# Kernel tuning notes

Measured on AMD Instinct MI355X. Metric: run time of the kernel, lower is better.

## Reference

```python
import jax, jax.numpy as jnp
import numpy as np

VOCAB_SIZE = 95
EMBED_DIM = 48
HIDDEN_DIM = 48


def setup_inputs() -> dict:
    key = jax.random.key(0)
    ks = jax.random.split(key, 8)
    B, S = 2048, 512
    x = jax.random.randint(ks[0], (B, S), 0, VOCAB_SIZE)
    s_e = 1.0  # torch Embedding default init ~ N(0,1); scale irrelevant for correctness
    emb = jax.random.normal(ks[1], (VOCAB_SIZE, EMBED_DIM), dtype=jnp.float32) * s_e
    k = 1.0 / np.sqrt(HIDDEN_DIM)
    w_ih = jax.random.uniform(ks[2], (3 * HIDDEN_DIM, EMBED_DIM), minval=-k, maxval=k, dtype=jnp.float32)
    w_hh = jax.random.uniform(ks[3], (3 * HIDDEN_DIM, HIDDEN_DIM), minval=-k, maxval=k, dtype=jnp.float32)
    b_ih = jax.random.uniform(ks[4], (3 * HIDDEN_DIM,), minval=-k, maxval=k, dtype=jnp.float32)
    b_hh = jax.random.uniform(ks[5], (3 * HIDDEN_DIM,), minval=-k, maxval=k, dtype=jnp.float32)
    w_out = jax.random.uniform(ks[6], (VOCAB_SIZE, HIDDEN_DIM), minval=-k, maxval=k, dtype=jnp.float32)
    b_out = jax.random.uniform(ks[7], (VOCAB_SIZE,), minval=-k, maxval=k, dtype=jnp.float32)
    return {"x": x, "emb": emb, "w_ih": w_ih, "w_hh": w_hh,
            "b_ih": b_ih, "b_hh": b_hh, "w_out": w_out, "b_out": b_out}


def _gru(embed, w_ih, w_hh, b_ih, b_hh):
    # embed: [B, S, E]. PyTorch GRU (single layer, batch_first):
    #   r = sig(Wir x + bir + Whr h + bhr); z = sig(Wiz x + biz + Whz h + bhz)
    B = embed.shape[0]
    H = w_hh.shape[1]
    # precompute input contributions for all timesteps: [S, B, 3H]
    xg = jnp.einsum('bse,ge->bsg', embed, w_ih) + b_ih
    xg = jnp.swapaxes(xg, 0, 1)
    h0 = jnp.zeros((B, H), dtype=embed.dtype)

    def step(h, xg_t):
        gh = h @ w_hh.T + b_hh  # [B, 3H]
        xr, xz, xn = jnp.split(xg_t, 3, axis=-1)
        hr, hz, hn = jnp.split(gh, 3, axis=-1)
        r = jax.nn.sigmoid(xr + hr)
        z = jax.nn.sigmoid(xz + hz)
        n = jnp.tanh(xn + r * hn)
        h_new = (1.0 - z) * n + z * h
        return h_new, h_new

    h_last, hs = jax.lax.scan(step, h0, xg)
    out = jnp.swapaxes(hs, 0, 1)  # [B, S, H]
    return out, h_last


def reference(x, emb, w_ih, w_hh, b_ih, b_hh, w_out, b_out):
    embed = emb[x]  # [B, S, E]
    out, h_last = _gru(embed, w_ih, w_hh, b_ih, b_hh)
    logits = jnp.einsum('bsh,vh->bsv', out, w_out) + b_out  # [B, S, V]
    hidden = h_last[None]  # [1, B, H] to match torch GRU hidden layout
    return logits, hidden
```

## Files before the change

### kernel.cpp

```cpp
#include <hip/hip_runtime.h>
#include <hip/hip_bf16.h>


#define BATCH 2048
#define SEQ   512
#define HDIM  48
#define VOCAB 95
#define G3    144

__device__ __forceinline__ float sigmoidf_(float x) {
    return 1.0f / (1.0f + __expf(-x));
}

__global__ void xg_precompute(const float* __restrict__ emb,
                              const float* __restrict__ w_ih,
                              const float* __restrict__ b_ih,
                              float* __restrict__ xg) {
    int v = blockIdx.x;
    int g = threadIdx.x;
    const float* e = emb + v * HDIM;
    const float* w = w_ih + g * HDIM;
    float a0 = 0.f, a1 = 0.f, a2 = 0.f, a3 = 0.f;
    #pragma unroll
    for (int k = 0; k < HDIM; k += 4) {
        a0 = fmaf(w[k + 0], e[k + 0], a0);
        a1 = fmaf(w[k + 1], e[k + 1], a1);
        a2 = fmaf(w[k + 2], e[k + 2], a2);
        a3 = fmaf(w[k + 3], e[k + 3], a3);
    }
    xg[v * G3 + g] = b_ih[g] + ((a0 + a1) + (a2 + a3));
}

__global__ __launch_bounds__(64, 2)
void gru_rec(const int* __restrict__ x,
             const float* __restrict__ xg_table,
             const float* __restrict__ w_hh,
             const float* __restrict__ b_hh,
             float* __restrict__ out,
             float* __restrict__ hidden) {
    const int row = blockIdx.x;
    const int j   = threadIdx.x;
    __shared__ float hsh[HDIM];

    float4 wr[12], wz[12], wn[12];
    float br = 0.f, bz = 0.f, bn = 0.f;
    float hj = 0.f;
    if (j < HDIM) {
        const float4* whr = (const float4*)(w_hh + (j         ) * HDIM);
        const float4* whz = (const float4*)(w_hh + (j +   HDIM) * HDIM);
        const float4* whn = (const float4*)(w_hh + (j + 2*HDIM) * HDIM);
        #pragma unroll
        for (int k = 0; k < 12; ++k) { wr[k] = whr[k]; wz[k] = whz[k]; wn[k] = whn[k]; }
        br = b_hh[j]; bz = b_hh[j + HDIM]; bn = b_hh[j + 2*HDIM];
        hsh[j] = 0.f;
    }
    __syncthreads();

    const int* xrow = x + row * SEQ;
    int tok = xrow[0];
    for (int t = 0; t < SEQ; ++t) {
        int tok_next = (t + 1 < SEQ) ? xrow[t + 1] : 0;
        float hnew = 0.f;
        if (j < HDIM) {
            const float* xg = xg_table + tok * G3;
            float xr = xg[j], xz = xg[j + HDIM], xn = xg[j + 2*HDIM];
            float accr = br, accz = bz, accn = bn;
            const float4* h4 = (const float4*)hsh;
            #pragma unroll
            for (int k = 0; k < 12; ++k) {
                float4 hh = h4[k];
                accr = fmaf(wr[k].x, hh.x, accr); accr = fmaf(wr[k].y, hh.y, accr);
                accr = fmaf(wr[k].z, hh.z, accr); accr = fmaf(wr[k].w, hh.w, accr);
                accz = fmaf(wz[k].x, hh.x, accz); accz = fmaf(wz[k].y, hh.y, accz);
                accz = fmaf(wz[k].z, hh.z, accz); accz = fmaf(wz[k].w, hh.w, accz);
                accn = fmaf(wn[k].x, hh.x, accn); accn = fmaf(wn[k].y, hh.y, accn);
                accn = fmaf(wn[k].z, hh.z, accn); accn = fmaf(wn[k].w, hh.w, accn);
            }
            float r = sigmoidf_(xr + accr);
            float z = sigmoidf_(xz + accz);
            float n = tanhf(xn + r * accn);
            hnew = (1.0f - z) * n + z * hj;
            hj = hnew;
            out[((long)(row * SEQ + t)) * VOCAB + j] = hnew;
        }
        __syncthreads();
        if (j < HDIM) hsh[j] = hnew;
        __syncthreads();
        tok = tok_next;
    }
    if (j < HDIM) hidden[row * HDIM + j] = hj;
}

__global__ __launch_bounds__(256, 2)
void logits_k(const float* __restrict__ w_out,
              const float* __restrict__ b_out,
              float* __restrict__ out) {
    __shared__ float hsh[256 * HDIM];
    const long pos0 = (long)blockIdx.x * 256;
    const int tid = threadIdx.x;

    for (int i = tid; i < 256 * HDIM; i += 256) {
        int p = i / HDIM;
        int k = i - p * HDIM;
        hsh[i] = out[(pos0 + p) * VOCAB + k];
    }
    __syncthreads();

    float h[HDIM];
    #pragma unroll
    for (int k = 0; k < 12; ++k)
        ((float4*)h)[k] = ((const float4*)(hsh + tid * HDIM))[k];

    float* orow = out + (pos0 + tid) * VOCAB;
    for (int v = 0; v < VOCAB; ++v) {
        const float* w = w_out + v * HDIM;
        float a0 = 0.f, a1 = 0.f, a2 = 0.f, a3 = 0.f;
        #pragma unroll
        for (int k = 0; k < HDIM; k += 4) {
            a0 = fmaf(w[k + 0], h[k + 0], a0);
            a1 = fmaf(w[k + 1], h[k + 1], a1);
            a2 = fmaf(w[k + 2], h[k + 2], a2);
            a3 = fmaf(w[k + 3], h[k + 3], a3);
        }
        orow[v] = b_out[v] + ((a0 + a1) + (a2 + a3));
    }
}

extern "C" void kernel_launch(void* const* d_in, const int* in_sizes, int n_in,
                              void* d_out, int out_size, void* d_ws, size_t ws_size,
                              hipStream_t stream) {
    const int*   x     = (const int*)d_in[0];
    const float* emb   = (const float*)d_in[1];
    const float* w_ih  = (const float*)d_in[2];
    const float* w_hh  = (const float*)d_in[3];
    const float* b_ih  = (const float*)d_in[4];
    const float* b_hh  = (const float*)d_in[5];
    const float* w_out = (const float*)d_in[6];
    const float* b_out = (const float*)d_in[7];

    float* out    = (float*)d_out;
    float* hidden = out + (long)BATCH * SEQ * VOCAB;
    float* xg     = (float*)d_ws;

    xg_precompute<<<VOCAB, G3, 0, stream>>>(emb, w_ih, b_ih, xg);
    gru_rec<<<BATCH, 64, 0, stream>>>(x, xg, w_hh, b_hh, out, hidden);
    logits_k<<<(BATCH * SEQ) / 256, 256, 0, stream>>>(w_out, b_out, out);
}
```

Baseline: 1.329 ms.

## Use wave barriers in GRU, prefetch gate inputs, tile logits with coalesced stores

The recurrent kernel, which runs a single 64-thread wave per row, now uses wave barriers instead of full block barriers. It also prefetches the next timestep's input-gate values ahead of the dependent recurrence math and swaps tanhf for an exp-based fast tanh. The logits kernel now processes 64 positions per block, with each wave computing a slice of the vocabulary. Results go to a shared-memory tile that is written back with coalesced float4 stores, replacing strided per-thread row writes. This risks more LDS use per block, and the fast tanh gives slightly different rounding.

```diff
diff --git a/kernel.cpp b/kernel.cpp
--- a/kernel.cpp
+++ b/kernel.cpp
@@ -7,9 +7,16 @@
 #define HDIM  48
 #define VOCAB 95
 #define G3    144
+#define HPAD  52
 
 __device__ __forceinline__ float sigmoidf_(float x) {
     return 1.0f / (1.0f + __expf(-x));
+}
+__device__ __forceinline__ float fast_tanh(float x) {
+    float ax = fabsf(x);
+    float e  = __expf(-2.0f * ax);
+    float r  = (1.0f - e) / (1.0f + e);
+    return copysignf(r, x);
 }
 
 __global__ void xg_precompute(const float* __restrict__ emb,
@@ -54,16 +61,26 @@
         br = b_hh[j]; bz = b_hh[j + HDIM]; bn = b_hh[j + 2*HDIM];
         hsh[j] = 0.f;
     }
-    __syncthreads();
+    __builtin_amdgcn_wave_barrier();
 
     const int* xrow = x + row * SEQ;
-    int tok = xrow[0];
+    float* orow = out + (long)row * SEQ * VOCAB + j;
+
+    int tok0 = xrow[0];
+    float xr = 0.f, xz = 0.f, xn = 0.f;
+    if (j < HDIM) {
+        const float* xg0 = xg_table + tok0 * G3;
+        xr = xg0[j]; xz = xg0[j + HDIM]; xn = xg0[j + 2*HDIM];
+    }
+
     for (int t = 0; t < SEQ; ++t) {
         int tok_next = (t + 1 < SEQ) ? xrow[t + 1] : 0;
+        const float* xgn = xg_table + tok_next * G3;
+        float xr_n = 0.f, xz_n = 0.f, xn_n = 0.f;
+        if (j < HDIM) { xr_n = xgn[j]; xz_n = xgn[j + HDIM]; xn_n = xgn[j + 2*HDIM]; }
+
         float hnew = 0.f;
         if (j < HDIM) {
-            const float* xg = xg_table + tok * G3;
-            float xr = xg[j], xz = xg[j + HDIM], xn = xg[j + 2*HDIM];
             float accr = br, accz = bz, accn = bn;
             const float4* h4 = (const float4*)hsh;
             #pragma unroll
@@ -78,52 +95,64 @@
             }
             float r = sigmoidf_(xr + accr);
             float z = sigmoidf_(xz + accz);
-            float n = tanhf(xn + r * accn);
+            float n = fast_tanh(xn + r * accn);
             hnew = (1.0f - z) * n + z * hj;
             hj = hnew;
-            out[((long)(row * SEQ + t)) * VOCAB + j] = hnew;
+            orow[(long)t * VOCAB] = hnew;
         }
-        __syncthreads();
+        __builtin_amdgcn_wave_barrier();
         if (j < HDIM) hsh[j] = hnew;
-        __syncthreads();
-        tok = tok_next;
+        __builtin_amdgcn_wave_barrier();
+        xr = xr_n; xz = xz_n; xn = xn_n;
     }
     if (j < HDIM) hidden[row * HDIM + j] = hj;
 }
 
-__global__ __launch_bounds__(256, 2)
+#define PTILE 64
+__global__ __launch_bounds__(256, 4)
 void logits_k(const float* __restrict__ w_out,
               const float* __restrict__ b_out,
               float* __restrict__ out) {
-    __shared__ float hsh[256 * HDIM];
-    const long pos0 = (long)blockIdx.x * 256;
+    __shared__ float hsh[PTILE * HPAD];
+    __shared__ float ltile[PTILE * VOCAB];
+    const long pos0 = (long)blockIdx.x * PTILE;
     const int tid = threadIdx.x;
 
-    for (int i = tid; i < 256 * HDIM; i += 256) {
+    for (int i = tid; i < PTILE * HDIM; i += 256) {
         int p = i / HDIM;
         int k = i - p * HDIM;
-        hsh[i] = out[(pos0 + p) * VOCAB + k];
+        hsh[p * HPAD + k] = out[(pos0 + p) * VOCAB + k];
     }
     __syncthreads();
+
+    const int lane = tid & 63;
+    const int w    = tid >> 6;
+    const int vstart = w * 24;
+    const int vend   = (vstart + 24 < VOCAB) ? vstart + 24 : VOCAB;
 
     float h[HDIM];
     #pragma unroll
     for (int k = 0; k < 12; ++k)
-        ((float4*)h)[k] = ((const float4*)(hsh + tid * HDIM))[k];
+        ((float4*)h)[k] = ((const float4*)(hsh + lane * HPAD))[k];
 
-    float* orow = out + (pos0 + tid) * VOCAB;
-    for (int v = 0; v < VOCAB; ++v) {
-        const float* w = w_out + v * HDIM;
+    for (int v = vstart; v < vend; ++v) {
+        const float* wv = w_out + v * HDIM;
         float a0 = 0.f, a1 = 0.f, a2 = 0.f, a3 = 0.f;
         #pragma unroll
         for (int k = 0; k < HDIM; k += 4) {
-            a0 = fmaf(w[k + 0], h[k + 0], a0);
-            a1 = fmaf(w[k + 1], h[k + 1], a1);
-            a2 = fmaf(w[k + 2], h[k + 2], a2);
-            a3 = fmaf(w[k + 3], h[k + 3], a3);
+            a0 = fmaf(wv[k + 0], h[k + 0], a0);
+            a1 = fmaf(wv[k + 1], h[k + 1], a1);
+            a2 = fmaf(wv[k + 2], h[k + 2], a2);
+            a3 = fmaf(wv[k + 3], h[k + 3], a3);
         }
-        orow[v] = b_out[v] + ((a0 + a1) + (a2 + a3));
+        ltile[lane * VOCAB + v] = b_out[v] + ((a0 + a1) + (a2 + a3));
     }
+    __syncthreads();
+
+    float4* dst = (float4*)(out + pos0 * VOCAB);
+    const float4* src = (const float4*)ltile;
+    for (int i = tid; i < (PTILE * VOCAB) / 4; i += 256)
+        dst[i] = src[i];
 }
 
 extern "C" void kernel_launch(void* const* d_in, const int* in_sizes, int n_in,
@@ -144,5 +173,5 @@
 
     xg_precompute<<<VOCAB, G3, 0, stream>>>(emb, w_ih, b_ih, xg);
     gru_rec<<<BATCH, 64, 0, stream>>>(x, xg, w_hh, b_hh, out, hidden);
-    logits_k<<<(BATCH * SEQ) / 256, 256, 0, stream>>>(w_out, b_out, out);
+    logits_k<<<(BATCH * SEQ) / PTILE, 256, 0, stream>>>(w_out, b_out, out);
 }
```

After: 2.273 ms. +71.1%, slower.
